# Optimization experiments

Hardware: AMD Instinct MI355X
Metric: run time of the kernel (lower is better)

## Reference

```python
import jax, jax.numpy as jnp
import numpy as np

NMS_THR = 0.3        # cfg.TEST.NMS
SCORE_THR = 0.5      # thr_2 == False branch
DEDUP_IOU_THR = 0.3  # compute_iou default iou_thresh


def _iou_matrix(a, b):
    # a: [N,4], b: [M,4] -> [N,M] IoU (matches compute_iou math: no +1, 1e-6 eps)
    area_a = (a[:, 2] - a[:, 0]) * (a[:, 3] - a[:, 1])
    area_b = (b[:, 2] - b[:, 0]) * (b[:, 3] - b[:, 1])
    lt = jnp.maximum(a[:, None, :2], b[None, :, :2])
    rb = jnp.minimum(a[:, None, 2:4], b[None, :, 2:4])
    wh = jnp.maximum(rb - lt, 0.0)
    inter = wh[..., 0] * wh[..., 1]
    return inter / (area_a[:, None] + area_b[None, :] - inter + 1e-6)


def _chan_norm(f):
    # f: [C,H,W] -> mean over channels, then Frobenius norm (torch.norm p=2)
    return jnp.linalg.norm(jnp.mean(f, axis=0))


def setup_inputs() -> dict:
    key = jax.random.key(0)
    ks = jax.random.split(key, 8)
    N, C, M = 2000, 21, 20

    def make_boxes(k, n, W=800.0, H=600.0):
        k1, k2, k3, k4 = jax.random.split(k, 4)
        cx = jax.random.uniform(k1, (n,)) * (W - 100.0) + 50.0
        cy = jax.random.uniform(k2, (n,)) * (H - 100.0) + 50.0
        w = jax.random.uniform(k3, (n,)) * 150.0 + 20.0
        h = jax.random.uniform(k4, (n,)) * 150.0 + 20.0
        return jnp.stack([cx - w / 2, cy - h / 2, cx + w / 2, cy + h / 2], -1)

    boxes = make_boxes(ks[0], N)
    rois = jnp.concatenate([jnp.zeros((N, 1)), boxes], -1)[None]
    cls_prob = jax.random.uniform(ks[1], (1, N, C))
    bbox_pred = 0.5 * jax.random.normal(ks[2], (1, N, 4 * C))
    im_info = jnp.array([[600.0, 800.0, 1.6]], jnp.float32)
    gt_b = make_boxes(ks[3], M)
    gt_lbl = jax.random.randint(ks[4], (M, 1), 1, C).astype(jnp.float32)
    gt_boxes = jnp.concatenate([gt_b, gt_lbl], -1)[None]
    feat = jax.random.normal(ks[5], (1, 512, 38, 50))
    feat_org = feat + 0.1 * jax.random.normal(ks[6], (1, 512, 38, 50))
    feat_res = 0.1 * jax.random.normal(ks[7], (1, 512, 38, 50))
    return dict(rois=rois, cls_prob=cls_prob, bbox_pred=bbox_pred,
                im_info=im_info, gt_boxes=gt_boxes, num_boxes=12,
                feat=feat, feat_org=feat_org, feat_res=feat_res)


def reference(rois, cls_prob, bbox_pred, im_info, gt_boxes, num_boxes,
              feat, feat_org, feat_res):
    N, C = cls_prob.shape[1], cls_prob.shape[2]
    M = gt_boxes.shape[1]
    scores = cls_prob[0]                       # [N,C]
    boxes = rois[0, :, 1:5]                    # [N,4]

    # bbox_transform_inv with BBOX_NORMALIZE_STDS/MEANS (means = 0)
    stds = jnp.array([0.1, 0.1, 0.2, 0.2], scores.dtype)
    deltas = bbox_pred[0].reshape(N, C, 4) * stds
    w = boxes[:, 2] - boxes[:, 0] + 1.0
    h = boxes[:, 3] - boxes[:, 1] + 1.0
    cx = boxes[:, 0] + 0.5 * w
    cy = boxes[:, 1] + 0.5 * h
    pcx = deltas[..., 0] * w[:, None] + cx[:, None]
    pcy = deltas[..., 1] * h[:, None] + cy[:, None]
    pw = jnp.exp(deltas[..., 2]) * w[:, None]
    ph = jnp.exp(deltas[..., 3]) * h[:, None]
    pred = jnp.stack([pcx - 0.5 * pw, pcy - 0.5 * ph,
                      pcx + 0.5 * pw, pcy + 0.5 * ph], -1)  # [N,C,4]
    H_im, W_im = im_info[0, 0], im_info[0, 1]
    pred = jnp.stack([jnp.clip(pred[..., 0], 0.0, W_im - 1),
                      jnp.clip(pred[..., 1], 0.0, H_im - 1),
                      jnp.clip(pred[..., 2], 0.0, W_im - 1),
                      jnp.clip(pred[..., 3], 0.0, H_im - 1)], -1)

    gt = gt_boxes[0]
    gt_valid = jnp.arange(M) < num_boxes
    idx = jnp.arange(N)

    def per_class(sj, bj):
        # score threshold + sort descending (invalid sorted last)
        valid = sj > SCORE_THR
        order = jnp.argsort(jnp.where(valid, -sj, jnp.inf))
        sb = bj[order]
        ss = sj[order]
        sv = valid[order]
        iou = _iou_matrix(sb, sb)              # [N,N]

        # greedy NMS over descending-score order
        def body(keep, i):
            sup = jnp.any(keep & (iou[i] > NMS_THR) & (idx < i))
            k = sv[i] & ~sup
            return keep.at[i].set(k), None
        keep, _ = jax.lax.scan(body, jnp.zeros(N, bool), idx)

        # dedup against valid gt boxes (vectorized replacement of the Python
        # double loop over compute_iou)
        gt_iou = _iou_matrix(sb, gt[:, :4])    # [N,M]
        hit = jnp.any((gt_iou > DEDUP_IOU_THR) & gt_valid[None, :], axis=1)
        final = keep & ~hit
        dets = jnp.concatenate([sb, ss[:, None]], -1)
        return dets * final[:, None].astype(dets.dtype)  # [N,5]

    # classes 1..C-1 (skip background), class-specific boxes
    dets = jax.vmap(per_class)(scores[:, 1:].T,
                               jnp.swapaxes(pred[:, 1:, :], 0, 1))  # [C-1,N,5]

    # feature distillation losses (L1 between scalar channel-mean norms)
    f, fo, fr = feat[0], feat_org[0], feat_res[0]
    n_f = _chan_norm(f)
    distil_loss = jnp.abs(n_f - _chan_norm(fo))
    res_loss = jnp.abs(_chan_norm(f - fo) - _chan_norm(fr))
    res_loss_inc = jnp.abs(_chan_norm(fo + fr) - n_f)
    residual_loss = res_loss_inc + res_loss

    return jnp.concatenate([dets.reshape(-1),
                            jnp.stack([distil_loss, residual_loss])])
```

## Files before the change

### kernel.cpp

```cpp
#include <hip/hip_runtime.h>
#include <hip/hip_bf16.h>

#pragma clang fp contract(off)

#define N_BOX 2000
#define N_CLS 21
#define SORT_N 2048
#define M_GT 20
#define FEAT_HW 1900
#define FEAT_F4 475
#define FEAT_C 512
#define BLK 1024
#define NW_MAX 22
#define IOU_GRID 2048

#define OFF_SBOX (32768)
#define OFF_SS   (32768 + 655360)
#define OFF_V    (851968)
#define OFF_BIT  (1048576)

__device__ __forceinline__ float bf2f(__hip_bfloat16 x) { return __bfloat162float(x); }
__device__ __forceinline__ float fin(float x) { return (x == x && fabsf(x) <= 3.0e38f) ? x : 0.0f; }
__device__ __forceinline__ bool probe_is_f32(const void* im_info) {
    return *(const unsigned*)im_info == 0x44160000u;
}
__device__ __forceinline__ float ld(const void* p, bool f32, int i) {
    return f32 ? ((const float*)p)[i] : bf2f(((const __hip_bfloat16*)p)[i]);
}
__device__ __forceinline__ float4 ld4f(const void* p, bool f32, int i4) {
    if (f32) return ((const float4*)p)[i4];
    ushort4 u = ((const ushort4*)p)[i4];
    return make_float4(__uint_as_float((unsigned)u.x << 16),
                       __uint_as_float((unsigned)u.y << 16),
                       __uint_as_float((unsigned)u.z << 16),
                       __uint_as_float((unsigned)u.w << 16));
}
__device__ __forceinline__ float iou_f(float4 a, float4 b) {
    float area_a = (a.z - a.x) * (a.w - a.y);
    float area_b = (b.z - b.x) * (b.w - b.y);
    float ltx = fmaxf(a.x, b.x), lty = fmaxf(a.y, b.y);
    float rbx = fminf(a.z, b.z), rby = fminf(a.w, b.w);
    float wx = fmaxf(rbx - ltx, 0.0f), wy = fmaxf(rby - lty, 0.0f);
    float inter = wx * wy;
    return inter / (area_a + area_b - inter + 1e-6f);
}
__device__ __forceinline__ int parse_count(const void* p) {
    int iv = *(const int*)p;
    if (iv >= 0 && iv <= 1000) return iv < M_GT ? iv : M_GT;
    float fv = *(const float*)p;
    if (fv >= 0.0f && fv <= 1000.0f) { int v = (int)fv; return v < M_GT ? v : M_GT; }
    float bv = bf2f(*(const __hip_bfloat16*)p);
    if (bv >= 0.0f && bv <= 1000.0f) { int v = (int)bv; return v < M_GT ? v : M_GT; }
    return 0;
}
__device__ __forceinline__ float4 decode_box(const void* rois, const void* bbox_pred,
                                             bool f32, int n, int c, float Wim, float Him) {
    float x1 = ld(rois, f32, n * 5 + 1);
    float y1 = ld(rois, f32, n * 5 + 2);
    float x2 = ld(rois, f32, n * 5 + 3);
    float y2 = ld(rois, f32, n * 5 + 4);
    float w = x2 - x1 + 1.0f;
    float h = y2 - y1 + 1.0f;
    float cx = x1 + 0.5f * w;
    float cy = y1 + 0.5f * h;
    int dbase = n * (4 * N_CLS) + c * 4;
    float d0, d1, d2, d3;
    if (f32) {
        float4 d = *(const float4*)((const float*)bbox_pred + dbase);
        d0 = d.x * 0.1f; d1 = d.y * 0.1f; d2 = d.z * 0.2f; d3 = d.w * 0.2f;
    } else {
        d0 = ld(bbox_pred, f32, dbase + 0) * 0.1f;
        d1 = ld(bbox_pred, f32, dbase + 1) * 0.1f;
        d2 = ld(bbox_pred, f32, dbase + 2) * 0.2f;
        d3 = ld(bbox_pred, f32, dbase + 3) * 0.2f;
    }
    float pcx = d0 * w + cx;
    float pcy = d1 * h + cy;
    float pw = (float)exp((double)d2) * w;
    float ph = (float)exp((double)d3) * h;
    float xmax = Wim - 1.0f, ymax = Him - 1.0f;
    float xa = fminf(fmaxf(pcx - 0.5f * pw, 0.0f), xmax);
    float ya = fminf(fmaxf(pcy - 0.5f * ph, 0.0f), ymax);
    float xb = fminf(fmaxf(pcx + 0.5f * pw, 0.0f), xmax);
    float yb = fminf(fmaxf(pcy + 0.5f * ph, 0.0f), ymax);
    return make_float4(fin(xa), fin(ya), fin(xb), fin(yb));
}
__device__ __forceinline__ unsigned long long readlane64(unsigned long long v, int l) {
    unsigned lo = (unsigned)__builtin_amdgcn_readlane((unsigned)(v & 0xFFFFFFFFull), l);
    unsigned hi = (unsigned)__builtin_amdgcn_readlane((unsigned)(v >> 32), l);
    return ((unsigned long long)hi << 32) | (unsigned long long)lo;
}

__global__ __launch_bounds__(BLK) void rank_loss_kernel(
        const void* __restrict__ rois, const void* __restrict__ cls_prob,
        const void* __restrict__ bbox_pred, const void* __restrict__ im_info,
        const void* __restrict__ feat, const void* __restrict__ feat_org,
        const void* __restrict__ feat_res,
        float4* __restrict__ wsbox, float* __restrict__ wss, int* __restrict__ wV,
        float* __restrict__ acc) {
    __shared__ unsigned long long keys[SORT_N];
    __shared__ float4 red[3][16][16];
    __shared__ int lds_V;
    const int tid = threadIdx.x;
    const int lane = tid & 63;
    const int wv = tid >> 6;
    const bool f32 = probe_is_f32(im_info);

    if (blockIdx.x >= 320) {
        const int lb = blockIdx.x - 320;
        const int fc = lb * 16 + (lane & 15);
        const int cg = (wv << 2) | (lane >> 4);
        float4 sa = make_float4(0.f, 0.f, 0.f, 0.f);
        float4 sb4 = make_float4(0.f, 0.f, 0.f, 0.f);
        float4 sr4 = make_float4(0.f, 0.f, 0.f, 0.f);
        if (fc < FEAT_F4) {
            #pragma unroll
            for (int k = 0; k < 8; ++k) {
                int off = ((cg << 3) + k) * FEAT_F4 + fc;
                float4 fa = ld4f(feat, f32, off);
                float4 fb = ld4f(feat_org, f32, off);
                float4 fc4 = ld4f(feat_res, f32, off);
                sa.x += fin(fa.x); sa.y += fin(fa.y); sa.z += fin(fa.z); sa.w += fin(fa.w);
                sb4.x += fin(fb.x); sb4.y += fin(fb.y); sb4.z += fin(fb.z); sb4.w += fin(fb.w);
                sr4.x += fin(fc4.x); sr4.y += fin(fc4.y); sr4.z += fin(fc4.z); sr4.w += fin(fc4.w);
            }
        }
        #pragma unroll
        for (int o = 16; o <= 32; o <<= 1) {
            sa.x += __shfl_xor(sa.x, o); sa.y += __shfl_xor(sa.y, o);
            sa.z += __shfl_xor(sa.z, o); sa.w += __shfl_xor(sa.w, o);
            sb4.x += __shfl_xor(sb4.x, o); sb4.y += __shfl_xor(sb4.y, o);
            sb4.z += __shfl_xor(sb4.z, o); sb4.w += __shfl_xor(sb4.w, o);
            sr4.x += __shfl_xor(sr4.x, o); sr4.y += __shfl_xor(sr4.y, o);
            sr4.z += __shfl_xor(sr4.z, o); sr4.w += __shfl_xor(sr4.w, o);
        }
        if (lane < 16) { red[0][wv][lane] = sa; red[1][wv][lane] = sb4; red[2][wv][lane] = sr4; }
        __syncthreads();
        if (wv == 0) {
            float4 ta = make_float4(0.f, 0.f, 0.f, 0.f);
            float4 tb = make_float4(0.f, 0.f, 0.f, 0.f);
            float4 tr = make_float4(0.f, 0.f, 0.f, 0.f);
            if (lane < 16) {
                #pragma unroll
                for (int w = 0; w < 16; ++w) {
                    float4 x = red[0][w][lane];
                    ta.x += x.x; ta.y += x.y; ta.z += x.z; ta.w += x.w;
                    x = red[1][w][lane];
                    tb.x += x.x; tb.y += x.y; tb.z += x.z; tb.w += x.w;
                    x = red[2][w][lane];
                    tr.x += x.x; tr.y += x.y; tr.z += x.z; tr.w += x.w;
                }
            }
            const float inv = 1.0f / 512.0f;
            float v0 = 0.f, v1 = 0.f, v2 = 0.f, v3 = 0.f, v4 = 0.f;
            {
                float ma, mb, mr;
                ma = ta.x * inv; mb = tb.x * inv; mr = tr.x * inv;
                v0 += ma * ma; v1 += mb * mb; v2 += (ma - mb) * (ma - mb);
                v3 += (mb + mr) * (mb + mr); v4 += mr * mr;
                ma = ta.y * inv; mb = tb.y * inv; mr = tr.y * inv;
                v0 += ma * ma; v1 += mb * mb; v2 += (ma - mb) * (ma - mb);
                v3 += (mb + mr) * (mb + mr); v4 += mr * mr;
                ma = ta.z * inv; mb = tb.z * inv; mr = tr.z * inv;
                v0 += ma * ma; v1 += mb * mb; v2 += (ma - mb) * (ma - mb);
                v3 += (mb + mr) * (mb + mr); v4 += mr * mr;
                ma = ta.w * inv; mb = tb.w * inv; mr = tr.w * inv;
                v0 += ma * ma; v1 += mb * mb; v2 += (ma - mb) * (ma - mb);
                v3 += (mb + mr) * (mb + mr); v4 += mr * mr;
            }
            for (int o = 32; o; o >>= 1) {
                v0 += __shfl_down(v0, o); v1 += __shfl_down(v1, o); v2 += __shfl_down(v2, o);
                v3 += __shfl_down(v3, o); v4 += __shfl_down(v4, o);
            }
            if (lane == 0) {
                float* part = acc + 64 + lb * 8;
                part[0] = v0; part[1] = v1; part[2] = v2; part[3] = v3; part[4] = v4;
            }
        }
        return;
    }

    const int cc = blockIdx.x >> 4;
    const int oct = blockIdx.x & 15;
    const int cls = cc + 1;
    if (tid == 0) lds_V = 0;
    __syncthreads();

    auto makekey = [&](int e) -> unsigned long long {
        if (e < N_BOX) {
            float s = ld(cls_prob, f32, e * N_CLS + cls);
            bool valid = s > 0.5f;
            float kf = valid ? -s : __builtin_inff();
            unsigned kbv = __float_as_uint(kf);
            kbv = (kbv & 0x80000000u) ? ~kbv : (kbv | 0x80000000u);
            return ((unsigned long long)kbv << 32) | (unsigned)e;
        }
        return ~0ull;
    };
    unsigned long long k0 = makekey(tid);
    unsigned long long k1 = makekey(tid + 1024);
    keys[tid] = k0;
    keys[tid + 1024] = k1;
    {
        unsigned long long m0 = __ballot((k0 >> 32) < 0xFF800000ull);
        unsigned long long m1 = __ballot((k1 >> 32) < 0xFF800000ull);
        if (lane == 0) {
            int vc = __popcll(m0) + __popcll(m1);
            if (vc) atomicAdd(&lds_V, vc);
        }
    }
    __syncthreads();
    if (oct == 0 && tid == 0) wV[cc] = lds_V;

    const int i = (oct << 7) + (tid >> 3);
    const int seg = tid & 7;
    const unsigned long long ki = keys[i];
    int rank = 0;
    #pragma unroll 8
    for (int jj = 0; jj < 256; ++jj) {
        rank += (keys[(jj << 3) | seg] < ki) ? 1 : 0;
    }
    rank += __shfl_xor(rank, 1);
    rank += __shfl_xor(rank, 2);
    rank += __shfl_xor(rank, 4);
    if (seg == 0 && i < N_BOX) {
        unsigned h = (unsigned)(ki >> 32);
        if (h < 0xFF800000u) {
            const float Him = fin(ld(im_info, f32, 0));
            const float Wim = fin(ld(im_info, f32, 1));
            wsbox[cc * SORT_N + rank] = decode_box(rois, bbox_pred, f32, i, cls, Wim, Him);
            wss[cc * SORT_N + rank] = -__uint_as_float(~h);
        }
    }
}

__global__ __launch_bounds__(256) void ioumat_kernel(
        const float4* __restrict__ wsbox, const int* __restrict__ wV,
        unsigned long long* __restrict__ bitmat,
        float* __restrict__ out, int out_n) {
    const int tid = threadIdx.x;
    const int bid = blockIdx.x;
    for (int i = bid * 256 + tid; i < out_n; i += IOU_GRID * 256) out[i] = 0.0f;

    int total = 0;
    #pragma unroll
    for (int c = 0; c < 20; ++c) {
        int nwc = (wV[c] + 63) >> 6;
        total += (nwc * (nwc + 1)) >> 1;
    }

    const int lane = tid & 63;
    const int wv = tid >> 6;

    for (int w = bid; w < total; w += IOU_GRID) {
        int cc = 0, t = 0, acc_t = 0;
        #pragma unroll
        for (int c = 0; c < 20; ++c) {
            int nwc = (wV[c] + 63) >> 6;
            int cnt = (nwc * (nwc + 1)) >> 1;
            if (w >= acc_t && w < acc_t + cnt) { cc = c; t = w - acc_t; }
            acc_t += cnt;
        }
        const int V = wV[cc];
        const int nw = (V + 63) >> 6;
        float mf = (float)(2 * nw + 1);
        int a = (int)((mf - sqrtf(fmaxf(mf * mf - 8.0f * (float)t, 0.0f))) * 0.5f);
        if (a < 0) a = 0;
        if (a > nw - 1) a = nw - 1;
        while (a + 1 <= nw - 1 && ((a + 1) * nw - (((a + 1) * a) >> 1)) <= t) ++a;
        while ((a * nw - ((a * (a - 1)) >> 1)) > t) --a;
        const int b = a + (t - (a * nw - ((a * (a - 1)) >> 1)));

        const float4* sb = wsbox + cc * SORT_N;
        unsigned long long* bm = bitmat + ((size_t)cc * SORT_N << 5);

        const int j = (b << 6) | lane;
        float4 bj = sb[j];
        const float aj = (bj.z - bj.x) * (bj.w - bj.y);
        const int rbase = (a << 6) + (wv << 4);
        #pragma unroll
        for (int rr = 0; rr < 16; ++rr) {
            const int r = rbase + rr;
            float4 bi = sb[r];
            float ai = (bi.z - bi.x) * (bi.w - bi.y);
            float ltx = fmaxf(bi.x, bj.x), lty = fmaxf(bi.y, bj.y);
            float rbx = fminf(bi.z, bj.z), rby = fminf(bi.w, bj.w);
            float wx = fmaxf(rbx - ltx, 0.0f), wy = fmaxf(rby - lty, 0.0f);
            float inter = wx * wy;
            float iou = inter / (ai + aj - inter + 1e-6f);
            bool conf = (j > r) && (j < V) && (iou > 0.3f);
            unsigned long long m = __ballot(conf);
            if (lane == 0 && r < V) bm[((size_t)r << 5) + b] = m;
        }
    }
}

__global__ __launch_bounds__(BLK) void scan_write_kernel(
        const void* __restrict__ im_info, const void* __restrict__ gt_boxes,
        const void* __restrict__ num_boxes,
        const float4* __restrict__ wsbox, const float* __restrict__ wss,
        const int* __restrict__ wV, const unsigned long long* __restrict__ bitmat,
        const float* __restrict__ acc, float* __restrict__ out) {
    __shared__ unsigned long long tri[16928];
    __shared__ unsigned long long diag_l[NW_MAX * 64];
    __shared__ unsigned long long keepw_s[32];
    __shared__ float4 gtb[M_GT];
    __shared__ int rb2_s[NW_MAX];
    __shared__ int len2_s[NW_MAX];
    const int tid = threadIdx.x;
    const int lane = tid & 63;
    const int wv = tid >> 6;
    const bool f32 = probe_is_f32(im_info);

    if (blockIdx.x == 20) {
        if (tid < 64) {
            float v0 = 0.f, v1 = 0.f, v2 = 0.f, v3 = 0.f, v4 = 0.f;
            if (tid < 30) {
                const float* p = acc + 64 + tid * 8;
                v0 = p[0]; v1 = p[1]; v2 = p[2]; v3 = p[3]; v4 = p[4];
            }
            for (int o = 32; o; o >>= 1) {
                v0 += __shfl_down(v0, o); v1 += __shfl_down(v1, o); v2 += __shfl_down(v2, o);
                v3 += __shfl_down(v3, o); v4 += __shfl_down(v4, o);
            }
            if (tid == 0) {
                float nA = sqrtf(fmaxf(fin(v0), 0.0f));
                float nB = sqrtf(fmaxf(fin(v1), 0.0f));
                float nAB = sqrtf(fmaxf(fin(v2), 0.0f));
                float nBR = sqrtf(fmaxf(fin(v3), 0.0f));
                float nR = sqrtf(fmaxf(fin(v4), 0.0f));
                float* out2 = out + (long)N_BOX * (N_CLS - 1) * 5;
                out2[0] = fin(fabsf(nA - nB));
                out2[1] = fin(fabsf(nBR - nA) + fabsf(nAB - nR));
            }
        }
        return;
    }

    const int cc = blockIdx.x;
    const int V = wV[cc];
    const int nw = (V + 63) >> 6;
    const unsigned long long* bm = bitmat + ((size_t)cc * SORT_N << 5);
    const bool planA = (V > 0) && (nw <= NW_MAX);
    if (tid < 32) keepw_s[tid] = 0ull;
    if (tid >= 64 && tid < 64 + M_GT) {
        int g = tid - 64;
        gtb[g] = make_float4(fin(ld(gt_boxes, f32, g * 5 + 0)),
                             fin(ld(gt_boxes, f32, g * 5 + 1)),
                             fin(ld(gt_boxes, f32, g * 5 + 2)),
                             fin(ld(gt_boxes, f32, g * 5 + 3)));
    }
    if (tid == 0) {
        int a = 0;
        for (int b = 0; b < NW_MAX; ++b) {
            rb2_s[b] = a;
            int b2 = b & ~1;
            int l2 = ((nw - b2) + 1) & ~1;
            if (l2 < 0) l2 = 0;
            len2_s[b] = l2;
            a += 64 * l2;
        }
    }
    __syncthreads();

    if (planA) {
        #pragma unroll 2
        for (int t = tid; t < (V << 4); t += BLK) {
            const int r = t >> 4;
            const int c = t & 15;
            const int b = r >> 6;
            const int b2 = b & ~1;
            const int l2 = len2_s[b];
            if ((c << 1) < l2) {
                ulonglong2 v = *(const ulonglong2*)(bm + ((size_t)r << 5) + b2 + (c << 1));
                const int idx = rb2_s[b] + (r & 63) * l2 + (c << 1);
                tri[idx] = v.x;
                tri[idx + 1] = v.y;
                if (c == 0) diag_l[r] = (b & 1) ? v.y : v.x;
            }
        }
    }
    __syncthreads();

    if (planA) {
        if (wv == 0) {
            const int wl = lane & 31;
            unsigned long long removedW = 0ull, keepW = 0ull;
            unsigned long long d_cur = diag_l[lane];
            for (int B = 0; B < nw; ++B) {
                unsigned long long d_nxt = (B + 1 < nw) ? diag_l[((B + 1) << 6) + lane] : 0ull;
                const int rbase = B << 6;
                int rows = V - rbase; if (rows > 64) rows = 64;
                const unsigned long long valid = (rows >= 64) ? ~0ull : ((1ull << rows) - 1ull);
                const unsigned long long curRem = readlane64(removedW, B);
                unsigned long long cand = ~curRem & valid;
                unsigned long long keepB = 0ull;
                while (cand) {
                    int r = __builtin_ctzll(cand);
                    keepB |= (1ull << r);
                    unsigned long long dr = readlane64(d_cur, r);
                    cand &= ~(dr | (1ull << r));
                }
                const int rbv = rb2_s[B];
                const int l2 = len2_s[B];
                const int wo = wl - (B & ~1);
                unsigned long long kk = keepB, add = 0ull;
                while (kk) {
                    int rr[8];
                    rr[0] = __builtin_ctzll(kk); kk &= kk - 1ull;
                    #pragma unroll
                    for (int t = 1; t < 8; ++t) {
                        rr[t] = kk ? __builtin_ctzll(kk) : rr[0];
                        if (kk) kk &= kk - 1ull;
                    }
                    unsigned long long a = 0ull;
                    #pragma unroll
                    for (int t = 0; t < 8; ++t)
                        a |= tri[rbv + rr[t] * l2 + wo];
                    add |= a;
                }
                removedW |= add;
                if (wl == B) keepW |= keepB;
                d_cur = d_nxt;
            }
            if (lane < 32) keepw_s[lane] = keepW;
        }
    } else if (V > 0) {
        if (wv == 0) {
            const int wl = lane & 31;
            unsigned long long removedW = 0ull, keepW = 0ull;
            unsigned long long d_cur = bm[((size_t)lane << 5)];
            for (int B = 0; B < nw; ++B) {
                unsigned long long d_nxt = 0ull;
                if (B + 1 < nw) {
                    int rn = ((B + 1) << 6) + lane;
                    d_nxt = bm[((size_t)rn << 5) + (B + 1)];
                }
                const int rbase = B << 6;
                int rows = V - rbase; if (rows > 64) rows = 64;
                const unsigned long long valid = (rows >= 64) ? ~0ull : ((1ull << rows) - 1ull);
                const unsigned long long curRem = readlane64(removedW, B);
                unsigned long long cand = ~curRem & valid;
                unsigned long long keepB = 0ull;
                while (cand) {
                    int r = __builtin_ctzll(cand);
                    keepB |= (1ull << r);
                    unsigned long long dr = readlane64(d_cur, r);
                    cand &= ~(dr | (1ull << r));
                }
                unsigned long long kk = keepB, add = 0ull;
                while (kk) {
                    int rr[8];
                    rr[0] = __builtin_ctzll(kk); kk &= kk - 1ull;
                    #pragma unroll
                    for (int t = 1; t < 8; ++t) {
                        rr[t] = kk ? __builtin_ctzll(kk) : rr[0];
                        if (kk) kk &= kk - 1ull;
                    }
                    unsigned long long a = 0ull;
                    #pragma unroll
                    for (int t = 0; t < 8; ++t)
                        a |= bm[((size_t)(rbase + rr[t]) << 5) + wl];
                    add |= a;
                }
                removedW |= add;
                if (wl == B) keepW |= keepB;
                d_cur = d_nxt;
            }
            if (lane < 32) keepw_s[lane] = keepW;
        }
    }
    __syncthreads();

    const int nb = parse_count(num_boxes);
    long obase = (long)cc * (N_BOX * 5);
    for (int i = tid; i < N_BOX; i += BLK) {
        if ((keepw_s[i >> 6] >> (i & 63)) & 1ull) {
            float4 b = wsbox[cc * SORT_N + i];
            bool fn = true;
            for (int m = 0; m < nb; ++m) {
                if (iou_f(b, gtb[m]) > 0.3f) { fn = false; break; }
            }
            if (fn) {
                float* op = out + obase + (long)i * 5;
                op[0] = b.x; op[1] = b.y; op[2] = b.z; op[3] = b.w; op[4] = wss[cc * SORT_N + i];
            }
        }
    }
}

extern "C" void kernel_launch(void* const* d_in, const int* in_sizes, int n_in,
                              void* d_out, int out_size, void* d_ws, size_t ws_size,
                              hipStream_t stream) {
    const void* p_rois = nullptr;
    const void* p_cls = nullptr;
    const void* p_bbox = nullptr;
    const void* p_iminfo = nullptr;
    const void* p_gt = nullptr;
    const void* p_nb = nullptr;
    const void* p_feat[3] = {nullptr, nullptr, nullptr};
    int nfeat = 0;
    for (int i = 0; i < n_in; ++i) {
        int s = in_sizes[i];
        if (s == 10000 || s == 20000) p_rois = d_in[i];
        else if (s == 42000 || s == 84000) p_cls = d_in[i];
        else if (s == 168000 || s == 336000) p_bbox = d_in[i];
        else if (s == 3 || s == 6) p_iminfo = d_in[i];
        else if (s == 100 || s == 200) p_gt = d_in[i];
        else if (s == 1 || s == 4) p_nb = d_in[i];
        else if ((s == 972800 || s == 1945600) && nfeat < 3) p_feat[nfeat++] = d_in[i];
    }
    if (!p_rois)   p_rois = d_in[0];
    if (!p_cls)    p_cls = d_in[1];
    if (!p_bbox)   p_bbox = d_in[2];
    if (!p_iminfo) p_iminfo = d_in[3];
    if (!p_gt)     p_gt = d_in[4];
    if (!p_nb)     p_nb = d_in[5];
    if (nfeat < 3) { p_feat[0] = d_in[6]; p_feat[1] = d_in[7]; p_feat[2] = d_in[8]; }

    float* out = (float*)d_out;
    char* ws = (char*)d_ws;
    float* acc = (float*)ws;

    float4* wsbox = (float4*)(ws + OFF_SBOX);
    float* wss = (float*)(ws + OFF_SS);
    int* wV = (int*)(ws + OFF_V);
    unsigned long long* bitmat = (unsigned long long*)(ws + OFF_BIT);

    rank_loss_kernel<<<350, BLK, 0, stream>>>(p_rois, p_cls, p_bbox, p_iminfo,
                                              p_feat[0], p_feat[1], p_feat[2],
                                              wsbox, wss, wV, acc);
    ioumat_kernel<<<IOU_GRID, 256, 0, stream>>>(wsbox, wV, bitmat, out, out_size);
    scan_write_kernel<<<21, BLK, 0, stream>>>(p_iminfo, p_gt, p_nb, wsbox, wss,
                                              wV, bitmat, acc, out);
}
```

Measured before the change: 156.2 us.

## Emit packed triangle bitmask from IoU kernel and pipeline its LDS staging with NMS scan

The IoU kernel now also writes each 64x64 suppression word into a packed per-class triangle layout in global workspace. The scan kernel can then copy that buffer contiguously into LDS pair by pair instead of gathering it from the strided bitmatrix in one upfront phase. Waves 1..15 prefetch the next block-pair while wave 0 runs the greedy NMS on the current pair, with a barrier per pair. This costs an extra global write stream and a larger workspace, and adds a __syncthreads per pair in the serial scan loop.

```diff
diff --git a/kernel.cpp b/kernel.cpp
--- a/kernel.cpp
+++ b/kernel.cpp
@@ -13,11 +13,13 @@
 #define BLK 1024
 #define NW_MAX 22
 #define IOU_GRID 2048
+#define TRI_U64 16928
 
 #define OFF_SBOX (32768)
 #define OFF_SS   (32768 + 655360)
 #define OFF_V    (851968)
 #define OFF_BIT  (1048576)
+#define OFF_TRI  (11534336)
 
 __device__ __forceinline__ float bf2f(__hip_bfloat16 x) { return __bfloat162float(x); }
 __device__ __forceinline__ float fin(float x) { return (x == x && fabsf(x) <= 3.0e38f) ? x : 0.0f; }
@@ -237,6 +239,7 @@
 __global__ __launch_bounds__(256) void ioumat_kernel(
         const float4* __restrict__ wsbox, const int* __restrict__ wV,
         unsigned long long* __restrict__ bitmat,
+        unsigned long long* __restrict__ triG,
         float* __restrict__ out, int out_n) {
     const int tid = threadIdx.x;
     const int bid = blockIdx.x;
@@ -271,8 +274,15 @@
         while ((a * nw - ((a * (a - 1)) >> 1)) > t) --a;
         const int b = a + (t - (a * nw - ((a * (a - 1)) >> 1)));
 
+        const int b2a = a & ~1;
+        const int l2a = ((nw - b2a) + 1) & ~1;
+        int rb2a = 0;
+        for (int pb = 0; pb < b2a; pb += 2) rb2a += 128 * (((nw - pb) + 1) & ~1);
+        if (a & 1) rb2a += 64 * l2a;
+
         const float4* sb = wsbox + cc * SORT_N;
         unsigned long long* bm = bitmat + ((size_t)cc * SORT_N << 5);
+        unsigned long long* trc = triG + (size_t)cc * TRI_U64;
 
         const int j = (b << 6) | lane;
         float4 bj = sb[j];
@@ -290,7 +300,10 @@
             float iou = inter / (ai + aj - inter + 1e-6f);
             bool conf = (j > r) && (j < V) && (iou > 0.3f);
             unsigned long long m = __ballot(conf);
-            if (lane == 0 && r < V) bm[((size_t)r << 5) + b] = m;
+            if (lane == 0 && r < V) {
+                bm[((size_t)r << 5) + b] = m;
+                trc[rb2a + (r & 63) * l2a + (b - b2a)] = m;
+            }
         }
     }
 }
@@ -300,9 +313,9 @@
         const void* __restrict__ num_boxes,
         const float4* __restrict__ wsbox, const float* __restrict__ wss,
         const int* __restrict__ wV, const unsigned long long* __restrict__ bitmat,
+        const unsigned long long* __restrict__ triG,
         const float* __restrict__ acc, float* __restrict__ out) {
-    __shared__ unsigned long long tri[16928];
-    __shared__ unsigned long long diag_l[NW_MAX * 64];
+    __shared__ unsigned long long tri[TRI_U64];
     __shared__ unsigned long long keepw_s[32];
     __shared__ float4 gtb[M_GT];
     __shared__ int rb2_s[NW_MAX];
@@ -341,6 +354,7 @@
     const int V = wV[cc];
     const int nw = (V + 63) >> 6;
     const unsigned long long* bm = bitmat + ((size_t)cc * SORT_N << 5);
+    const unsigned long long* trG = triG + (size_t)cc * TRI_U64;
     const bool planA = (V > 0) && (nw <= NW_MAX);
     if (tid < 32) keepw_s[tid] = 0ull;
     if (tid >= 64 && tid < 64 + M_GT) {
@@ -364,67 +378,71 @@
     __syncthreads();
 
     if (planA) {
-        #pragma unroll 2
-        for (int t = tid; t < (V << 4); t += BLK) {
-            const int r = t >> 4;
-            const int c = t & 15;
-            const int b = r >> 6;
-            const int b2 = b & ~1;
-            const int l2 = len2_s[b];
-            if ((c << 1) < l2) {
-                ulonglong2 v = *(const ulonglong2*)(bm + ((size_t)r << 5) + b2 + (c << 1));
-                const int idx = rb2_s[b] + (r & 63) * l2 + (c << 1);
-                tri[idx] = v.x;
-                tri[idx + 1] = v.y;
-                if (c == 0) diag_l[r] = (b & 1) ? v.y : v.x;
-            }
-        }
-    }
-    __syncthreads();
-
-    if (planA) {
-        if (wv == 0) {
-            const int wl = lane & 31;
-            unsigned long long removedW = 0ull, keepW = 0ull;
-            unsigned long long d_cur = diag_l[lane];
-            for (int B = 0; B < nw; ++B) {
-                unsigned long long d_nxt = (B + 1 < nw) ? diag_l[((B + 1) << 6) + lane] : 0ull;
-                const int rbase = B << 6;
-                int rows = V - rbase; if (rows > 64) rows = 64;
-                const unsigned long long valid = (rows >= 64) ? ~0ull : ((1ull << rows) - 1ull);
-                const unsigned long long curRem = readlane64(removedW, B);
-                unsigned long long cand = ~curRem & valid;
-                unsigned long long keepB = 0ull;
-                while (cand) {
-                    int r = __builtin_ctzll(cand);
-                    keepB |= (1ull << r);
-                    unsigned long long dr = readlane64(d_cur, r);
-                    cand &= ~(dr | (1ull << r));
+        const int PAIRS = (nw + 1) >> 1;
+        auto prefetch_pair = [&](int p, int tlo, int tcnt) {
+            const int b2 = p << 1;
+            const int l2 = len2_s[b2];
+            const int base = rb2_s[b2];
+            int rows = V - (b2 << 6); if (rows > 128) rows = 128;
+            if (rows <= 0 || l2 <= 0) return;
+            const int nu2 = (rows * l2) >> 1;
+            for (int i = tlo; i < nu2; i += tcnt) {
+                ulonglong2 v = *(const ulonglong2*)(trG + base + (i << 1));
+                *(ulonglong2*)(tri + base + (i << 1)) = v;
+            }
+        };
+        prefetch_pair(0, tid, BLK);
+        __syncthreads();
+
+        const int wl = lane & 31;
+        unsigned long long removedW = 0ull, keepW = 0ull;
+        for (int p = 0; p < PAIRS; ++p) {
+            if (wv > 0) {
+                if (p + 1 < PAIRS) prefetch_pair(p + 1, tid - 64, BLK - 64);
+            } else {
+                #pragma unroll
+                for (int h = 0; h < 2; ++h) {
+                    const int B = (p << 1) + h;
+                    if (B >= nw) break;
+                    const int rbase = B << 6;
+                    if (rbase >= V) break;
+                    const int rbv = rb2_s[B];
+                    const int l2 = len2_s[B];
+                    unsigned long long d_cur = tri[rbv + lane * l2 + (B & 1)];
+                    int rows = V - rbase; if (rows > 64) rows = 64;
+                    const unsigned long long valid = (rows >= 64) ? ~0ull : ((1ull << rows) - 1ull);
+                    const unsigned long long curRem = readlane64(removedW, B);
+                    unsigned long long cand = ~curRem & valid;
+                    unsigned long long keepB = 0ull;
+                    while (cand) {
+                        int r = __builtin_ctzll(cand);
+                        keepB |= (1ull << r);
+                        unsigned long long dr = readlane64(d_cur, r);
+                        cand &= ~(dr | (1ull << r));
+                    }
+                    const int wo = wl - (B & ~1);
+                    unsigned long long kk = keepB, add = 0ull;
+                    while (kk) {
+                        int rr[8];
+                        rr[0] = __builtin_ctzll(kk); kk &= kk - 1ull;
+                        #pragma unroll
+                        for (int t = 1; t < 8; ++t) {
+                            rr[t] = kk ? __builtin_ctzll(kk) : rr[0];
+                            if (kk) kk &= kk - 1ull;
+                        }
+                        unsigned long long a = 0ull;
+                        #pragma unroll
+                        for (int t = 0; t < 8; ++t)
+                            a |= tri[rbv + rr[t] * l2 + wo];
+                        add |= a;
+                    }
+                    removedW |= add;
+                    if (wl == B) keepW |= keepB;
                 }
-                const int rbv = rb2_s[B];
-                const int l2 = len2_s[B];
-                const int wo = wl - (B & ~1);
-                unsigned long long kk = keepB, add = 0ull;
-                while (kk) {
-                    int rr[8];
-                    rr[0] = __builtin_ctzll(kk); kk &= kk - 1ull;
-                    #pragma unroll
-                    for (int t = 1; t < 8; ++t) {
-                        rr[t] = kk ? __builtin_ctzll(kk) : rr[0];
-                        if (kk) kk &= kk - 1ull;
-                    }
-                    unsigned long long a = 0ull;
-                    #pragma unroll
-                    for (int t = 0; t < 8; ++t)
-                        a |= tri[rbv + rr[t] * l2 + wo];
-                    add |= a;
-                }
-                removedW |= add;
-                if (wl == B) keepW |= keepB;
-                d_cur = d_nxt;
-            }
-            if (lane < 32) keepw_s[lane] = keepW;
-        }
+            }
+            __syncthreads();
+        }
+        if (wv == 0 && lane < 32) keepw_s[lane] = keepW;
     } else if (V > 0) {
         if (wv == 0) {
             const int wl = lane & 31;
@@ -526,11 +544,12 @@
     float* wss = (float*)(ws + OFF_SS);
     int* wV = (int*)(ws + OFF_V);
     unsigned long long* bitmat = (unsigned long long*)(ws + OFF_BIT);
+    unsigned long long* triG = (unsigned long long*)(ws + OFF_TRI);
 
     rank_loss_kernel<<<350, BLK, 0, stream>>>(p_rois, p_cls, p_bbox, p_iminfo,
                                               p_feat[0], p_feat[1], p_feat[2],
                                               wsbox, wss, wV, acc);
-    ioumat_kernel<<<IOU_GRID, 256, 0, stream>>>(wsbox, wV, bitmat, out, out_size);
+    ioumat_kernel<<<IOU_GRID, 256, 0, stream>>>(wsbox, wV, bitmat, triG, out, out_size);
     scan_write_kernel<<<21, BLK, 0, stream>>>(p_iminfo, p_gt, p_nb, wsbox, wss,
-                                              wV, bitmat, acc, out);
-}
+                                              wV, bitmat, triG, acc, out);
+}
```

Measured after the change: 164.7 us. +5.5%, slower.

## Store transposed diagonal conflict masks and resolve intra-block NMS with ballots

Applied to the files above, without the earlier changes.

The IoU kernel now also writes, for each diagonal 64x64 tile, a column-transposed conflict mask, built by reducing per-wave partial masks through shared memory. The scan kernel loads these columns, and its serial intra-block NMS loop uses one ballot per kept box over per-lane removed flags, replacing the per-row readlane chain. The aim is to shorten the latency of the sequential greedy scan. In exchange, diagonal tiles in the IoU kernel take extra barriers and global writes, and more workspace is used.

```diff
diff --git a/kernel.cpp b/kernel.cpp
--- a/kernel.cpp
+++ b/kernel.cpp
@@ -18,6 +18,7 @@
 #define OFF_SS   (32768 + 655360)
 #define OFF_V    (851968)
 #define OFF_BIT  (1048576)
+#define OFF_DIAG (11534336)
 
 __device__ __forceinline__ float bf2f(__hip_bfloat16 x) { return __bfloat162float(x); }
 __device__ __forceinline__ float fin(float x) { return (x == x && fabsf(x) <= 3.0e38f) ? x : 0.0f; }
@@ -237,7 +238,9 @@
 __global__ __launch_bounds__(256) void ioumat_kernel(
         const float4* __restrict__ wsbox, const int* __restrict__ wV,
         unsigned long long* __restrict__ bitmat,
+        unsigned long long* __restrict__ diagT,
         float* __restrict__ out, int out_n) {
+    __shared__ unsigned long long colred[4][64];
     const int tid = threadIdx.x;
     const int bid = blockIdx.x;
     for (int i = bid * 256 + tid; i < out_n; i += IOU_GRID * 256) out[i] = 0.0f;
@@ -270,6 +273,7 @@
         while (a + 1 <= nw - 1 && ((a + 1) * nw - (((a + 1) * a) >> 1)) <= t) ++a;
         while ((a * nw - ((a * (a - 1)) >> 1)) > t) --a;
         const int b = a + (t - (a * nw - ((a * (a - 1)) >> 1)));
+        const bool diag = (a == b);
 
         const float4* sb = wsbox + cc * SORT_N;
         unsigned long long* bm = bitmat + ((size_t)cc * SORT_N << 5);
@@ -278,6 +282,7 @@
         float4 bj = sb[j];
         const float aj = (bj.z - bj.x) * (bj.w - bj.y);
         const int rbase = (a << 6) + (wv << 4);
+        unsigned long long colpart = 0ull;
         #pragma unroll
         for (int rr = 0; rr < 16; ++rr) {
             const int r = rbase + rr;
@@ -291,6 +296,17 @@
             bool conf = (j > r) && (j < V) && (iou > 0.3f);
             unsigned long long m = __ballot(conf);
             if (lane == 0 && r < V) bm[((size_t)r << 5) + b] = m;
+            if (diag) colpart |= conf ? (1ull << (r & 63)) : 0ull;
+        }
+        if (diag) {
+            __syncthreads();
+            colred[wv][lane] = colpart;
+            __syncthreads();
+            if (wv == 0) {
+                unsigned long long col = colred[0][lane] | colred[1][lane]
+                                       | colred[2][lane] | colred[3][lane];
+                diagT[(size_t)cc * SORT_N + (a << 6) + lane] = col;
+            }
         }
     }
 }
@@ -300,6 +316,7 @@
         const void* __restrict__ num_boxes,
         const float4* __restrict__ wsbox, const float* __restrict__ wss,
         const int* __restrict__ wV, const unsigned long long* __restrict__ bitmat,
+        const unsigned long long* __restrict__ diagT,
         const float* __restrict__ acc, float* __restrict__ out) {
     __shared__ unsigned long long tri[16928];
     __shared__ unsigned long long diag_l[NW_MAX * 64];
@@ -376,9 +393,10 @@
                 const int idx = rb2_s[b] + (r & 63) * l2 + (c << 1);
                 tri[idx] = v.x;
                 tri[idx + 1] = v.y;
-                if (c == 0) diag_l[r] = (b & 1) ? v.y : v.x;
-            }
-        }
+            }
+        }
+        for (int i = tid; i < (nw << 6); i += BLK)
+            diag_l[i] = diagT[(size_t)cc * SORT_N + i];
     }
     __syncthreads();
 
@@ -386,20 +404,21 @@
         if (wv == 0) {
             const int wl = lane & 31;
             unsigned long long removedW = 0ull, keepW = 0ull;
-            unsigned long long d_cur = diag_l[lane];
             for (int B = 0; B < nw; ++B) {
-                unsigned long long d_nxt = (B + 1 < nw) ? diag_l[((B + 1) << 6) + lane] : 0ull;
                 const int rbase = B << 6;
+                if (rbase >= V) break;
                 int rows = V - rbase; if (rows > 64) rows = 64;
                 const unsigned long long valid = (rows >= 64) ? ~0ull : ((1ull << rows) - 1ull);
                 const unsigned long long curRem = readlane64(removedW, B);
-                unsigned long long cand = ~curRem & valid;
+                const unsigned long long mcol = diag_l[rbase + lane];
+                bool remf = ((curRem >> lane) & 1ull) != 0ull;
+                unsigned long long cand = ~__ballot(remf) & valid;
                 unsigned long long keepB = 0ull;
                 while (cand) {
                     int r = __builtin_ctzll(cand);
-                    keepB |= (1ull << r);
-                    unsigned long long dr = readlane64(d_cur, r);
-                    cand &= ~(dr | (1ull << r));
+                    keepB |= 1ull << r;
+                    remf |= ((mcol >> r) & 1ull) != 0ull;
+                    cand = ~__ballot(remf) & valid & ((0xFFFFFFFFFFFFFFFEull) << r);
                 }
                 const int rbv = rb2_s[B];
                 const int l2 = len2_s[B];
@@ -421,7 +440,6 @@
                 }
                 removedW |= add;
                 if (wl == B) keepW |= keepB;
-                d_cur = d_nxt;
             }
             if (lane < 32) keepw_s[lane] = keepW;
         }
@@ -526,11 +544,12 @@
     float* wss = (float*)(ws + OFF_SS);
     int* wV = (int*)(ws + OFF_V);
     unsigned long long* bitmat = (unsigned long long*)(ws + OFF_BIT);
+    unsigned long long* diagT = (unsigned long long*)(ws + OFF_DIAG);
 
     rank_loss_kernel<<<350, BLK, 0, stream>>>(p_rois, p_cls, p_bbox, p_iminfo,
                                               p_feat[0], p_feat[1], p_feat[2],
                                               wsbox, wss, wV, acc);
-    ioumat_kernel<<<IOU_GRID, 256, 0, stream>>>(wsbox, wV, bitmat, out, out_size);
+    ioumat_kernel<<<IOU_GRID, 256, 0, stream>>>(wsbox, wV, bitmat, diagT, out, out_size);
     scan_write_kernel<<<21, BLK, 0, stream>>>(p_iminfo, p_gt, p_nb, wsbox, wss,
-                                              wV, bitmat, acc, out);
-}
+                                              wV, bitmat, diagT, acc, out);
+}
```

Result: no change. 156.2 us (+0.0%).

## Fuse IoU bitmask computation into per-class scan kernel using LDS

Applied to the files above, without the earlier changes.

Removes the separate IoU-matrix kernel and computes the suppression bitmask inside the per-class scan kernel, with sorted boxes staged in LDS and tiles written straight to the LDS triangle. This drops the global bitmat round-trip and one kernel launch. The cost is that all IoU work for a class now runs on a single 1024-thread block, 21 blocks in total, instead of being spread over 2048 blocks. Output zeroing moves into the rank kernel, and the diagonal greedy scan switches to a ballot-based column form.

```diff
diff --git a/kernel.cpp b/kernel.cpp
--- a/kernel.cpp
+++ b/kernel.cpp
@@ -11,8 +11,8 @@
 #define FEAT_F4 475
 #define FEAT_C 512
 #define BLK 1024
-#define NW_MAX 22
-#define IOU_GRID 2048
+#define NW_MAX 20
+#define TRI_LDS 14080
 
 #define OFF_SBOX (32768)
 #define OFF_SS   (32768 + 655360)
@@ -90,6 +90,16 @@
     unsigned hi = (unsigned)__builtin_amdgcn_readlane((unsigned)(v >> 32), l);
     return ((unsigned long long)hi << 32) | (unsigned long long)lo;
 }
+__device__ __forceinline__ void decode_ab(int t, int nw, int& a_out, int& b_out) {
+    float mf = (float)(2 * nw + 1);
+    int a = (int)((mf - sqrtf(fmaxf(mf * mf - 8.0f * (float)t, 0.0f))) * 0.5f);
+    if (a < 0) a = 0;
+    if (a > nw - 1) a = nw - 1;
+    while (a + 1 <= nw - 1 && ((a + 1) * nw - (((a + 1) * a) >> 1)) <= t) ++a;
+    while ((a * nw - ((a * (a - 1)) >> 1)) > t) --a;
+    a_out = a;
+    b_out = a + (t - (a * nw - ((a * (a - 1)) >> 1)));
+}
 
 __global__ __launch_bounds__(BLK) void rank_loss_kernel(
         const void* __restrict__ rois, const void* __restrict__ cls_prob,
@@ -97,7 +107,7 @@
         const void* __restrict__ feat, const void* __restrict__ feat_org,
         const void* __restrict__ feat_res,
         float4* __restrict__ wsbox, float* __restrict__ wss, int* __restrict__ wV,
-        float* __restrict__ acc) {
+        float* __restrict__ acc, float* __restrict__ out, int out_n) {
     __shared__ unsigned long long keys[SORT_N];
     __shared__ float4 red[3][16][16];
     __shared__ int lds_V;
@@ -105,6 +115,7 @@
     const int lane = tid & 63;
     const int wv = tid >> 6;
     const bool f32 = probe_is_f32(im_info);
+    for (int i = blockIdx.x * BLK + tid; i < out_n; i += 350 * BLK) out[i] = 0.0f;
 
     if (blockIdx.x >= 320) {
         const int lb = blockIdx.x - 320;
@@ -234,74 +245,14 @@
     }
 }
 
-__global__ __launch_bounds__(256) void ioumat_kernel(
-        const float4* __restrict__ wsbox, const int* __restrict__ wV,
-        unsigned long long* __restrict__ bitmat,
-        float* __restrict__ out, int out_n) {
-    const int tid = threadIdx.x;
-    const int bid = blockIdx.x;
-    for (int i = bid * 256 + tid; i < out_n; i += IOU_GRID * 256) out[i] = 0.0f;
-
-    int total = 0;
-    #pragma unroll
-    for (int c = 0; c < 20; ++c) {
-        int nwc = (wV[c] + 63) >> 6;
-        total += (nwc * (nwc + 1)) >> 1;
-    }
-
-    const int lane = tid & 63;
-    const int wv = tid >> 6;
-
-    for (int w = bid; w < total; w += IOU_GRID) {
-        int cc = 0, t = 0, acc_t = 0;
-        #pragma unroll
-        for (int c = 0; c < 20; ++c) {
-            int nwc = (wV[c] + 63) >> 6;
-            int cnt = (nwc * (nwc + 1)) >> 1;
-            if (w >= acc_t && w < acc_t + cnt) { cc = c; t = w - acc_t; }
-            acc_t += cnt;
-        }
-        const int V = wV[cc];
-        const int nw = (V + 63) >> 6;
-        float mf = (float)(2 * nw + 1);
-        int a = (int)((mf - sqrtf(fmaxf(mf * mf - 8.0f * (float)t, 0.0f))) * 0.5f);
-        if (a < 0) a = 0;
-        if (a > nw - 1) a = nw - 1;
-        while (a + 1 <= nw - 1 && ((a + 1) * nw - (((a + 1) * a) >> 1)) <= t) ++a;
-        while ((a * nw - ((a * (a - 1)) >> 1)) > t) --a;
-        const int b = a + (t - (a * nw - ((a * (a - 1)) >> 1)));
-
-        const float4* sb = wsbox + cc * SORT_N;
-        unsigned long long* bm = bitmat + ((size_t)cc * SORT_N << 5);
-
-        const int j = (b << 6) | lane;
-        float4 bj = sb[j];
-        const float aj = (bj.z - bj.x) * (bj.w - bj.y);
-        const int rbase = (a << 6) + (wv << 4);
-        #pragma unroll
-        for (int rr = 0; rr < 16; ++rr) {
-            const int r = rbase + rr;
-            float4 bi = sb[r];
-            float ai = (bi.z - bi.x) * (bi.w - bi.y);
-            float ltx = fmaxf(bi.x, bj.x), lty = fmaxf(bi.y, bj.y);
-            float rbx = fminf(bi.z, bj.z), rby = fminf(bi.w, bj.w);
-            float wx = fmaxf(rbx - ltx, 0.0f), wy = fmaxf(rby - lty, 0.0f);
-            float inter = wx * wy;
-            float iou = inter / (ai + aj - inter + 1e-6f);
-            bool conf = (j > r) && (j < V) && (iou > 0.3f);
-            unsigned long long m = __ballot(conf);
-            if (lane == 0 && r < V) bm[((size_t)r << 5) + b] = m;
-        }
-    }
-}
-
-__global__ __launch_bounds__(BLK) void scan_write_kernel(
+__global__ __launch_bounds__(BLK) void iou_scan_kernel(
         const void* __restrict__ im_info, const void* __restrict__ gt_boxes,
         const void* __restrict__ num_boxes,
         const float4* __restrict__ wsbox, const float* __restrict__ wss,
-        const int* __restrict__ wV, const unsigned long long* __restrict__ bitmat,
+        const int* __restrict__ wV, unsigned long long* __restrict__ bitmat,
         const float* __restrict__ acc, float* __restrict__ out) {
-    __shared__ unsigned long long tri[16928];
+    __shared__ unsigned long long tri[TRI_LDS];
+    __shared__ float4 sbl[SORT_N];
     __shared__ unsigned long long diag_l[NW_MAX * 64];
     __shared__ unsigned long long keepw_s[32];
     __shared__ float4 gtb[M_GT];
@@ -340,7 +291,6 @@
     const int cc = blockIdx.x;
     const int V = wV[cc];
     const int nw = (V + 63) >> 6;
-    const unsigned long long* bm = bitmat + ((size_t)cc * SORT_N << 5);
     const bool planA = (V > 0) && (nw <= NW_MAX);
     if (tid < 32) keepw_s[tid] = 0ull;
     if (tid >= 64 && tid < 64 + M_GT) {
@@ -361,22 +311,70 @@
             a += 64 * l2;
         }
     }
+    for (int i = tid; i < NW_MAX * 64; i += BLK) diag_l[i] = 0ull;
+    for (int i = tid; i < (nw << 6); i += BLK) sbl[i] = wsbox[cc * SORT_N + i];
     __syncthreads();
 
+    const int ntiles = (nw * (nw + 1)) >> 1;
+    const int nunits = ntiles << 2;
     if (planA) {
-        #pragma unroll 2
-        for (int t = tid; t < (V << 4); t += BLK) {
-            const int r = t >> 4;
-            const int c = t & 15;
-            const int b = r >> 6;
-            const int b2 = b & ~1;
-            const int l2 = len2_s[b];
-            if ((c << 1) < l2) {
-                ulonglong2 v = *(const ulonglong2*)(bm + ((size_t)r << 5) + b2 + (c << 1));
-                const int idx = rb2_s[b] + (r & 63) * l2 + (c << 1);
-                tri[idx] = v.x;
-                tri[idx + 1] = v.y;
-                if (c == 0) diag_l[r] = (b & 1) ? v.y : v.x;
+        for (int u = wv; u < nunits; u += 16) {
+            int a, b;
+            decode_ab(u >> 2, nw, a, b);
+            const int q = u & 3;
+            const int b2a = a & ~1;
+            const int l2a = len2_s[a];
+            const int rbva = rb2_s[a];
+            const int wo = b - b2a;
+            const int j = (b << 6) | lane;
+            float4 bj = sbl[j];
+            const float aj = (bj.z - bj.x) * (bj.w - bj.y);
+            const int rbase = (a << 6) + (q << 4);
+            unsigned long long colpart = 0ull;
+            #pragma unroll
+            for (int rr = 0; rr < 16; ++rr) {
+                const int r = rbase + rr;
+                float4 bi = sbl[r];
+                float ai = (bi.z - bi.x) * (bi.w - bi.y);
+                float ltx = fmaxf(bi.x, bj.x), lty = fmaxf(bi.y, bj.y);
+                float rbx = fminf(bi.z, bj.z), rby = fminf(bi.w, bj.w);
+                float wx = fmaxf(rbx - ltx, 0.0f), wy = fmaxf(rby - lty, 0.0f);
+                float inter = wx * wy;
+                float iou = inter / (ai + aj - inter + 1e-6f);
+                bool conf = (j > r) && (j < V) && (iou > 0.3f);
+                unsigned long long m = __ballot(conf);
+                if (lane == 0 && r < V) tri[rbva + (r & 63) * l2a + wo] = m;
+                if (a == b) colpart |= conf ? (1ull << (r & 63)) : 0ull;
+            }
+            if (a == b) {
+                unsigned* d32 = (unsigned*)&diag_l[(a << 6) + lane];
+                unsigned part = (unsigned)(colpart >> ((q >> 1) * 32));
+                if (part) atomicOr(&d32[q >> 1], part);
+            }
+        }
+    } else if (V > 0) {
+        unsigned long long* bm = bitmat + ((size_t)cc * SORT_N << 5);
+        for (int u = wv; u < nunits; u += 16) {
+            int a, b;
+            decode_ab(u >> 2, nw, a, b);
+            const int q = u & 3;
+            const int j = (b << 6) | lane;
+            float4 bj = sbl[j];
+            const float aj = (bj.z - bj.x) * (bj.w - bj.y);
+            const int rbase = (a << 6) + (q << 4);
+            #pragma unroll
+            for (int rr = 0; rr < 16; ++rr) {
+                const int r = rbase + rr;
+                float4 bi = sbl[r];
+                float ai = (bi.z - bi.x) * (bi.w - bi.y);
+                float ltx = fmaxf(bi.x, bj.x), lty = fmaxf(bi.y, bj.y);
+                float rbx = fminf(bi.z, bj.z), rby = fminf(bi.w, bj.w);
+                float wx = fmaxf(rbx - ltx, 0.0f), wy = fmaxf(rby - lty, 0.0f);
+                float inter = wx * wy;
+                float iou = inter / (ai + aj - inter + 1e-6f);
+                bool conf = (j > r) && (j < V) && (iou > 0.3f);
+                unsigned long long m = __ballot(conf);
+                if (lane == 0 && r < V) bm[((size_t)r << 5) + b] = m;
             }
         }
     }
@@ -386,20 +384,21 @@
         if (wv == 0) {
             const int wl = lane & 31;
             unsigned long long removedW = 0ull, keepW = 0ull;
-            unsigned long long d_cur = diag_l[lane];
             for (int B = 0; B < nw; ++B) {
-                unsigned long long d_nxt = (B + 1 < nw) ? diag_l[((B + 1) << 6) + lane] : 0ull;
                 const int rbase = B << 6;
+                if (rbase >= V) break;
                 int rows = V - rbase; if (rows > 64) rows = 64;
                 const unsigned long long valid = (rows >= 64) ? ~0ull : ((1ull << rows) - 1ull);
                 const unsigned long long curRem = readlane64(removedW, B);
-                unsigned long long cand = ~curRem & valid;
+                const unsigned long long mcol = diag_l[rbase + lane];
+                bool remf = ((curRem >> lane) & 1ull) != 0ull;
+                unsigned long long cand = ~__ballot(remf) & valid;
                 unsigned long long keepB = 0ull;
                 while (cand) {
                     int r = __builtin_ctzll(cand);
-                    keepB |= (1ull << r);
-                    unsigned long long dr = readlane64(d_cur, r);
-                    cand &= ~(dr | (1ull << r));
+                    keepB |= 1ull << r;
+                    remf |= ((mcol >> r) & 1ull) != 0ull;
+                    cand = ~__ballot(remf) & valid & ((0xFFFFFFFFFFFFFFFEull) << r);
                 }
                 const int rbv = rb2_s[B];
                 const int l2 = len2_s[B];
@@ -421,12 +420,12 @@
                 }
                 removedW |= add;
                 if (wl == B) keepW |= keepB;
-                d_cur = d_nxt;
             }
             if (lane < 32) keepw_s[lane] = keepW;
         }
     } else if (V > 0) {
         if (wv == 0) {
+            const unsigned long long* bm = bitmat + ((size_t)cc * SORT_N << 5);
             const int wl = lane & 31;
             unsigned long long removedW = 0ull, keepW = 0ull;
             unsigned long long d_cur = bm[((size_t)lane << 5)];
@@ -473,19 +472,19 @@
     __syncthreads();
 
     const int nb = parse_count(num_boxes);
-    long obase = (long)cc * (N_BOX * 5);
+    const long obase = (long)cc * (N_BOX * 5);
     for (int i = tid; i < N_BOX; i += BLK) {
+        float o0 = 0.f, o1 = 0.f, o2 = 0.f, o3 = 0.f, o4 = 0.f;
         if ((keepw_s[i >> 6] >> (i & 63)) & 1ull) {
-            float4 b = wsbox[cc * SORT_N + i];
+            float4 b = (i < (nw << 6)) ? sbl[i] : wsbox[cc * SORT_N + i];
             bool fn = true;
             for (int m = 0; m < nb; ++m) {
                 if (iou_f(b, gtb[m]) > 0.3f) { fn = false; break; }
             }
-            if (fn) {
-                float* op = out + obase + (long)i * 5;
-                op[0] = b.x; op[1] = b.y; op[2] = b.z; op[3] = b.w; op[4] = wss[cc * SORT_N + i];
-            }
-        }
+            if (fn) { o0 = b.x; o1 = b.y; o2 = b.z; o3 = b.w; o4 = wss[cc * SORT_N + i]; }
+        }
+        float* op = out + obase + (long)i * 5;
+        op[0] = o0; op[1] = o1; op[2] = o2; op[3] = o3; op[4] = o4;
     }
 }
 
@@ -529,8 +528,7 @@
 
     rank_loss_kernel<<<350, BLK, 0, stream>>>(p_rois, p_cls, p_bbox, p_iminfo,
                                               p_feat[0], p_feat[1], p_feat[2],
-                                              wsbox, wss, wV, acc);
-    ioumat_kernel<<<IOU_GRID, 256, 0, stream>>>(wsbox, wV, bitmat, out, out_size);
-    scan_write_kernel<<<21, BLK, 0, stream>>>(p_iminfo, p_gt, p_nb, wsbox, wss,
-                                              wV, bitmat, acc, out);
-}
+                                              wsbox, wss, wV, acc, out, out_size);
+    iou_scan_kernel<<<21, BLK, 0, stream>>>(p_iminfo, p_gt, p_nb, wsbox, wss,
+                                            wV, bitmat, acc, out);
+}
```

After: 308.9 us. 1.98x slower.
